# Performance work log

Hardware: AMD Instinct MI355X
Metric: run time of the kernel (lower is better)

## Reference

```python
import jax, jax.numpy as jnp
import numpy as np

EPS = 1e-6
N_HEADS, N_POINTS = 6, 4


def layer_norm(x, w, b):
    m = jnp.mean(x, -1, keepdims=True)
    v = jnp.mean((x - m) ** 2, -1, keepdims=True)
    return (x - m) * jax.lax.rsqrt(v + EPS) * w + b


def bilinear_sample(val, loc, Hl, Wl):
    # val: (B, nH, Hl*Wl, d); loc: (B, Lq, nH, P, 2) in [0,1]
    # matches F.grid_sample(mode='bilinear', padding='zeros', align_corners=False)
    B, nH, _, d = val.shape
    Lq, P = loc.shape[1], loc.shape[3]
    x = loc[..., 0] * Wl - 0.5
    y = loc[..., 1] * Hl - 0.5
    x0 = jnp.floor(x)
    y0 = jnp.floor(y)
    wx1 = x - x0
    wy1 = y - y0
    out = jnp.zeros((B, nH, Lq * P, d), val.dtype)
    corners = ((0, 0, (1 - wy1) * (1 - wx1)), (0, 1, (1 - wy1) * wx1),
               (1, 0, wy1 * (1 - wx1)), (1, 1, wy1 * wx1))
    for dy, dx, w in corners:
        xi = x0 + dx
        yi = y0 + dy
        valid = (xi >= 0) & (xi < Wl) & (yi >= 0) & (yi < Hl)
        xi_c = jnp.clip(xi, 0, Wl - 1).astype(jnp.int32)
        yi_c = jnp.clip(yi, 0, Hl - 1).astype(jnp.int32)
        idx = (yi_c * Wl + xi_c).transpose(0, 2, 1, 3).reshape(B, nH, Lq * P)
        g = jnp.take_along_axis(val, idx[..., None], axis=2)  # (B,nH,Lq*P,d)
        ww = jnp.where(valid, w, 0.0).transpose(0, 2, 1, 3).reshape(B, nH, Lq * P)
        out = out + g * ww[..., None]
    return out.reshape(B, nH, Lq, P, d).transpose(0, 2, 1, 3, 4)  # (B,Lq,nH,P,d)


def dwconv3x3(x, w, b):
    # x: (N, C, H, W); w: (C, 1, 3, 3) depthwise
    y = jax.lax.conv_general_dilated(x, w, (1, 1), 'SAME',
                                     feature_group_count=w.shape[0],
                                     dimension_numbers=('NCHW', 'OIHW', 'NCHW'))
    return y + b[None, :, None, None]


def setup_inputs() -> dict:
    key = jax.random.key(0)
    ks = jax.random.split(key, 16)
    B, H, W, C = 8, 32, 32, 768
    Lq = 3 * H * W
    Hf = Wf = 64
    hidden = int(C * 0.25)
    s = 0.02
    inp = {
        'query': jax.random.normal(ks[0], (B, Lq, C), jnp.float32),
        'reference_points': jax.random.uniform(ks[1], (B, Lq, 1, 2), jnp.float32),
        'feat': jax.random.normal(ks[2], (B, Hf * Wf, C), jnp.float32),
        'spatial_shapes': jnp.array([[Hf, Wf]], jnp.int32),
        'level_start_index': jnp.zeros((1,), jnp.int32),
        'H': H, 'W': W,
        'qn_w': jnp.ones((C,)), 'qn_b': jnp.zeros((C,)),
        'fn_w': jnp.ones((C,)), 'fn_b': jnp.zeros((C,)),
        'so_w': jax.random.normal(ks[3], (C, N_HEADS * N_POINTS * 2)) * s,
        'so_b': jax.random.normal(ks[4], (N_HEADS * N_POINTS * 2,)) * s,
        'aw_w': jax.random.normal(ks[5], (C, N_HEADS * N_POINTS)) * s,
        'aw_b': jnp.zeros((N_HEADS * N_POINTS,)),
        'vp_w': jax.random.normal(ks[6], (C, C)) * s,
        'vp_b': jnp.zeros((C,)),
        'op_w': jax.random.normal(ks[7], (C, C)) * s,
        'op_b': jnp.zeros((C,)),
        'ffn_w': jnp.ones((C,)), 'ffn_b': jnp.zeros((C,)),
        'fc1_w': jax.random.normal(ks[8], (C, hidden)) * s,
        'fc1_b': jnp.zeros((hidden,)),
        'dw_w': jax.random.normal(ks[9], (hidden, 1, 3, 3)) * s,
        'dw_b': jnp.zeros((hidden,)),
        'fc2_w': jax.random.normal(ks[10], (hidden, C)) * s,
        'fc2_b': jnp.zeros((C,)),
    }
    return inp


def reference(query, reference_points, feat, spatial_shapes, level_start_index, H, W,
              qn_w, qn_b, fn_w, fn_b, so_w, so_b, aw_w, aw_b, vp_w, vp_b, op_w, op_b,
              ffn_w, ffn_b, fc1_w, fc1_b, dw_w, dw_b, fc2_w, fc2_b):
    B, Lq, C = query.shape
    nH, nP = N_HEADS, N_POINTS
    d = C // nH
    ss = np.asarray(spatial_shapes)
    Hl, Wl = int(ss[0, 0]), int(ss[0, 1])

    # --- MSDeformAttn (single level) ---
    q = layer_norm(query, qn_w, qn_b)
    f = layer_norm(feat, fn_w, fn_b)
    value = (f @ vp_w + vp_b).reshape(B, Hl * Wl, nH, d).transpose(0, 2, 1, 3)  # (B,nH,Lin,d)
    offs = (q @ so_w + so_b).reshape(B, Lq, nH, 1, nP, 2)
    aw = jax.nn.softmax((q @ aw_w + aw_b).reshape(B, Lq, nH, nP), axis=-1)
    normalizer = jnp.array([Wl, Hl], query.dtype)
    loc = reference_points[:, :, None, :, None, :] + offs / normalizer  # (B,Lq,nH,1,nP,2)
    sampled = bilinear_sample(value, loc[:, :, :, 0], Hl, Wl)           # (B,Lq,nH,nP,d)
    attn = (sampled * aw[..., None]).sum(3).reshape(B, Lq, C) @ op_w + op_b
    query = query + attn

    # --- ConvFFN (3 equal HxW chunks through shared depthwise conv) ---
    x = layer_norm(query, ffn_w, ffn_b) @ fc1_w + fc1_b  # (B, 3*H*W, hid)
    n = Lq // 3
    hid = fc1_w.shape[1]
    xc = x.reshape(B, 3, n, hid).transpose(0, 1, 3, 2).reshape(B * 3, hid, H, W)
    xc = dwconv3x3(xc, dw_w, dw_b)
    x = xc.reshape(B, 3, hid, n).transpose(0, 1, 3, 2).reshape(B, Lq, hid)
    x = jax.nn.gelu(x, approximate=False)
    x = x @ fc2_w + fc2_b
    return query + x
```

## Files before the change

### kernel.cpp

```cpp
#include <hip/hip_runtime.h>
#include <hip/hip_bf16.h>
#include <math.h>

typedef __hip_bfloat16 bf16;
typedef short bf16x8 __attribute__((ext_vector_type(8)));
typedef short bf16x4 __attribute__((ext_vector_type(4)));
typedef float f32x4 __attribute__((ext_vector_type(4)));

#define NB 8
#define LQ 3072
#define CC 768
#define NHEADS 6
#define NPTS 4
#define DHEAD 128
#define HLVL 64
#define WLVL 64
#define LIN 4096
#define HID 192
#define BLTOT 24576
#define FROWS 32768

__device__ __forceinline__ float bf2f(short u)
{ return __uint_as_float(((unsigned)(unsigned short)u) << 16); }

__global__ __launch_bounds__(256)
void ln_bf16_kernel(const float* __restrict__ x, const float* __restrict__ w,
                    const float* __restrict__ b, bf16* __restrict__ out)
{
    const int row = blockIdx.x;
    const int t = threadIdx.x;
    const float* xr = x + (size_t)row * CC;
    float v0 = xr[t], v1 = xr[t + 256], v2 = xr[t + 512];
    float s = v0 + v1 + v2;
    float ss = v0 * v0 + v1 * v1 + v2 * v2;
    #pragma unroll
    for (int o = 32; o > 0; o >>= 1) {
        s += __shfl_down(s, o);
        ss += __shfl_down(ss, o);
    }
    __shared__ float red[8];
    const int lane = t & 63, wv = t >> 6;
    if (lane == 0) { red[wv] = s; red[4 + wv] = ss; }
    __syncthreads();
    if (t == 0) {
        float S = red[0] + red[1] + red[2] + red[3];
        float SS = red[4] + red[5] + red[6] + red[7];
        float m = S * (1.f / CC);
        float var = SS * (1.f / CC) - m * m;
        red[0] = m; red[1] = rsqrtf(var + 1e-6f);
    }
    __syncthreads();
    const float m = red[0], rs = red[1];
    bf16* o = out + (size_t)row * CC;
    o[t]       = __float2bfloat16((v0 - m) * rs * w[t] + b[t]);
    o[t + 256] = __float2bfloat16((v1 - m) * rs * w[t + 256] + b[t + 256]);
    o[t + 512] = __float2bfloat16((v2 - m) * rs * w[t + 512] + b[t + 512]);
}

__global__ __launch_bounds__(256)
void ln_bf16in_kernel(const bf16* __restrict__ x, const float* __restrict__ w,
                      const float* __restrict__ b, bf16* __restrict__ out)
{
    const int row = blockIdx.x * 4 + (threadIdx.x >> 6);
    const int lane = threadIdx.x & 63;
    const bf16* xr = x + (size_t)row * CC;
    bf16x8 v8 = *(const bf16x8*)(xr + lane * 8);
    bf16x4 v4 = *(const bf16x4*)(xr + 512 + lane * 4);
    float v[12];
    #pragma unroll
    for (int j = 0; j < 8; ++j) v[j] = bf2f(v8[j]);
    #pragma unroll
    for (int j = 0; j < 4; ++j) v[8 + j] = bf2f(v4[j]);
    float s = 0.f, ss = 0.f;
    #pragma unroll
    for (int j = 0; j < 12; ++j) { s += v[j]; ss += v[j] * v[j]; }
    #pragma unroll
    for (int o = 32; o > 0; o >>= 1) {
        s += __shfl_down(s, o);
        ss += __shfl_down(ss, o);
    }
    s = __shfl(s, 0); ss = __shfl(ss, 0);
    const float m = s * (1.f / CC);
    const float rs = rsqrtf(ss * (1.f / CC) - m * m + 1e-6f);
    float wv[12], bv[12];
    *(float4*)&wv[0] = *(const float4*)&w[lane * 8];
    *(float4*)&wv[4] = *(const float4*)&w[lane * 8 + 4];
    *(float4*)&wv[8] = *(const float4*)&w[512 + lane * 4];
    *(float4*)&bv[0] = *(const float4*)&b[lane * 8];
    *(float4*)&bv[4] = *(const float4*)&b[lane * 8 + 4];
    *(float4*)&bv[8] = *(const float4*)&b[512 + lane * 4];
    bf16 o8[8], o4[4];
    #pragma unroll
    for (int j = 0; j < 8; ++j) o8[j] = __float2bfloat16((v[j] - m) * rs * wv[j] + bv[j]);
    #pragma unroll
    for (int j = 0; j < 4; ++j) o4[j] = __float2bfloat16((v[8 + j] - m) * rs * wv[8 + j] + bv[8 + j]);
    bf16* orow = out + (size_t)row * CC;
    *(bf16x8*)(orow + lane * 8) = *(bf16x8*)o8;
    *(bf16x4*)(orow + 512 + lane * 4) = *(bf16x4*)o4;
}

__global__ __launch_bounds__(256)
void wt_bf16_kernel(const float* __restrict__ src, bf16* __restrict__ dst, int K, int N)
{
    __shared__ float t[64][65];
    const int tn0 = blockIdx.x * 64, tk0 = blockIdx.y * 64;
    const int r = threadIdx.x >> 6, c = threadIdx.x & 63;
    #pragma unroll
    for (int i = 0; i < 16; ++i) {
        const int k = i * 4 + r;
        t[k][c] = src[(size_t)(tk0 + k) * N + tn0 + c];
    }
    __syncthreads();
    #pragma unroll
    for (int i = 0; i < 16; ++i) {
        const int n = i * 4 + r;
        dst[(size_t)(tn0 + n) * K + tk0 + c] = __float2bfloat16(t[c][n]);
    }
}

__global__ __launch_bounds__(256)
void build_dots_w(const float* __restrict__ so_w, const float* __restrict__ so_b,
                  const float* __restrict__ aw_w, const float* __restrict__ aw_b,
                  bf16* __restrict__ wt, float* __restrict__ db)
{
    int i = blockIdx.x * 256 + threadIdx.x;
    if (i < 128 * 768) {
        int n = i / 768, k = i - n * 768;
        float v = 0.f;
        if (n < 48) v = so_w[(size_t)k * 48 + n];
        else if (n < 72) v = aw_w[(size_t)k * 24 + (n - 48)];
        wt[i] = __float2bfloat16(v);
    }
    if (i < 128) {
        float bv = 0.f;
        if (i < 48) bv = so_b[i];
        else if (i < 72) bv = aw_b[i - 48];
        db[i] = bv;
    }
}

template<int N_>
__device__ __forceinline__ void wait_vmcnt()
{
    if constexpr (N_ == 0)      asm volatile("s_waitcnt vmcnt(0)" ::: "memory");
    else if constexpr (N_ == 4) asm volatile("s_waitcnt vmcnt(4)" ::: "memory");
    else if constexpr (N_ == 5) asm volatile("s_waitcnt vmcnt(5)" ::: "memory");
    else if constexpr (N_ == 6) asm volatile("s_waitcnt vmcnt(6)" ::: "memory");
    else if constexpr (N_ == 8) asm volatile("s_waitcnt vmcnt(8)" ::: "memory");
    else static_assert(N_ == 0, "add a vmcnt case");
}

template<int BM, int BN, int WM, int WN, int MODE>
__global__ __launch_bounds__(256)
void gemm_kernel(const bf16* __restrict__ A, const bf16* __restrict__ Bt,
                 const float* __restrict__ bias, const void* __restrict__ resv,
                 void* __restrict__ outv, int M, int N, int K)
{
    constexpr int WAVES_N = BN / WN;
    constexpr int FM = WM / 16, FN = WN / 16;
    constexpr int CWA = BM / 32;
    constexpr int CWB = BN / 32;
    constexpr int LPT = CWA + CWB;
    constexpr int ABYTES = BM * 256;
    constexpr int DBUF_BYTES = (BM + BN) * 256;
    constexpr int EPI_BYTES = BM * BN * 4;
    constexpr size_t SMEM_BYTES = DBUF_BYTES > EPI_BYTES ? DBUF_BYTES : EPI_BYTES;
    __shared__ __align__(16) char smem[SMEM_BYTES];
    bf16* sA = (bf16*)smem;
    bf16* sB = (bf16*)(smem + ABYTES);
    float* epi = (float*)smem;

    const int tid = threadIdx.x;
    const int lane = tid & 63;
    const int wave = tid >> 6;

    const int nwgx = gridDim.x;
    const int nwg = nwgx * gridDim.y;
    const int bid = blockIdx.y * nwgx + blockIdx.x;
    const int swz = (bid & 7) * (nwg >> 3) + (bid >> 3);
    const int m0 = (swz / nwgx) * BM;
    const int n0 = (swz % nwgx) * BN;

    const int wm = (wave / WAVES_N) * WM;
    const int wn = (wave % WAVES_N) * WN;

    const int srow = lane >> 3;
    const int scol = ((lane & 7) ^ srow) * 8;

    constexpr int GPR8 = BN / 8;
    constexpr int GPT8 = (BM * BN / 8) / 256;
    constexpr int QPR4 = BN / 4;
    constexpr int QPT4 = (BM * BN / 4) / 256;
    float4 pr0[GPT8], pr1[GPT8];
    bf16x4 prb[QPT4];
    if constexpr (MODE == 3) {
        const float* resf = (const float*)resv;
        #pragma unroll
        for (int k = 0; k < GPT8; ++k) {
            const int f = k * 256 + tid;
            const int rr = f / GPR8, cc = (f % GPR8) * 8;
            const size_t gidx = (size_t)(m0 + rr) * N + n0 + cc;
            pr0[k] = *(const float4*)&resf[gidx];
            pr1[k] = *(const float4*)&resf[gidx + 4];
        }
    }
    if constexpr (MODE == 4) {
        const bf16* resb = (const bf16*)resv;
        #pragma unroll
        for (int k = 0; k < QPT4; ++k) {
            const int f = k * 256 + tid;
            const int rr = f / QPR4, cc = (f % QPR4) * 4;
            prb[k] = *(const bf16x4*)&resb[(size_t)(m0 + rr) * N + n0 + cc];
        }
    }

#define STAGE(tt, half)                                                                            \
    { const int k0_ = (tt) * 64;                                                                   \
      _Pragma("unroll")                                                                            \
      for (int i_ = 0; i_ < CWA; ++i_) {                                                           \
        const int c_ = i_ * 4 + wave;                                                              \
        __builtin_amdgcn_global_load_lds(                                                          \
          (const __attribute__((address_space(1))) void*)(A + (size_t)(m0 + c_ * 8 + srow) * K + k0_ + scol), \
          (__attribute__((address_space(3))) void*)(sA + (half) * (BM * 64) + c_ * 512), 16, 0, 0); } \
      _Pragma("unroll")                                                                            \
      for (int i_ = 0; i_ < CWB; ++i_) {                                                           \
        const int c_ = i_ * 4 + wave;                                                              \
        __builtin_amdgcn_global_load_lds(                                                          \
          (const __attribute__((address_space(1))) void*)(Bt + (size_t)(n0 + c_ * 8 + srow) * K + k0_ + scol), \
          (__attribute__((address_space(3))) void*)(sB + (half) * (BN * 64) + c_ * 512), 16, 0, 0); } }

    f32x4 acc[FM][FN] = {};
    const int nt = K >> 6;

    STAGE(0, 0);
    STAGE(1, 1);

    for (int t = 0; t < nt; ++t) {
        const int half = t & 1;
        if (t + 1 < nt) wait_vmcnt<LPT>();
        else            wait_vmcnt<0>();
        __builtin_amdgcn_s_barrier();
        const bf16* cA = sA + half * (BM * 64);
        const bf16* cB = sB + half * (BN * 64);
        #pragma unroll
        for (int kki = 0; kki < 2; ++kki) {
            const int kslot = kki * 4 + (lane >> 4);
            bf16x8 aF[FM], bF[FN];
            #pragma unroll
            for (int i = 0; i < FM; ++i) {
                const int row = wm + i * 16 + (lane & 15);
                aF[i] = *(const bf16x8*)(&cA[row * 64 + ((kslot ^ (row & 7)) * 8)]);
            }
            #pragma unroll
            for (int j = 0; j < FN; ++j) {
                const int row = wn + j * 16 + (lane & 15);
                bF[j] = *(const bf16x8*)(&cB[row * 64 + ((kslot ^ (row & 7)) * 8)]);
            }
            #pragma unroll
            for (int i = 0; i < FM; ++i) {
                #pragma unroll
                for (int j = 0; j < FN; ++j)
                    acc[i][j] = __builtin_amdgcn_mfma_f32_16x16x32_bf16(aF[i], bF[j], acc[i][j], 0, 0, 0);
            }
        }
        asm volatile("s_waitcnt lgkmcnt(0)" ::: "memory");
        __builtin_amdgcn_s_barrier();
        if (t + 2 < nt) STAGE(t + 2, half);
    }
#undef STAGE

    #pragma unroll
    for (int j = 0; j < FN; ++j) {
        const int colL = wn + j * 16 + (lane & 15);
        const float bj = bias[n0 + colL];
        #pragma unroll
        for (int i = 0; i < FM; ++i) {
            #pragma unroll
            for (int r = 0; r < 4; ++r) {
                const int rowL = wm + i * 16 + ((lane >> 4) << 2) + r;
                const int addr = rowL * BN + ((((colL >> 2) ^ (rowL & 7)) << 2) | (colL & 3));
                epi[addr] = acc[i][j][r] + bj;
            }
        }
    }
    __syncthreads();

    if constexpr (MODE == 0 || MODE == 3) {
        #pragma unroll
        for (int k = 0; k < GPT8; ++k) {
            const int f = k * 256 + tid;
            const int rr = f / GPR8, cc = (f % GPR8) * 8;
            const int g0 = ((cc >> 2) ^ (rr & 7)) << 2;
            const int g1 = (((cc >> 2) + 1) ^ (rr & 7)) << 2;
            float4 v0 = *(const float4*)&epi[rr * BN + g0];
            float4 v1 = *(const float4*)&epi[rr * BN + g1];
            if constexpr (MODE == 3) {
                v0.x += pr0[k].x; v0.y += pr0[k].y; v0.z += pr0[k].z; v0.w += pr0[k].w;
                v1.x += pr1[k].x; v1.y += pr1[k].y; v1.z += pr1[k].z; v1.w += pr1[k].w;
            }
            bf16 tmp[8];
            tmp[0] = __float2bfloat16(v0.x); tmp[1] = __float2bfloat16(v0.y);
            tmp[2] = __float2bfloat16(v0.z); tmp[3] = __float2bfloat16(v0.w);
            tmp[4] = __float2bfloat16(v1.x); tmp[5] = __float2bfloat16(v1.y);
            tmp[6] = __float2bfloat16(v1.z); tmp[7] = __float2bfloat16(v1.w);
            *(bf16x8*)((bf16*)outv + (size_t)(m0 + rr) * N + n0 + cc) = *(bf16x8*)tmp;
        }
    } else {
        #pragma unroll
        for (int k = 0; k < QPT4; ++k) {
            const int f = k * 256 + tid;
            const int rr = f / QPR4, cc = (f % QPR4) * 4;
            const int gs = ((cc >> 2) ^ (rr & 7)) << 2;
            float4 v = *(const float4*)&epi[rr * BN + gs];
            if constexpr (MODE == 4) {
                v.x += bf2f(prb[k][0]); v.y += bf2f(prb[k][1]);
                v.z += bf2f(prb[k][2]); v.w += bf2f(prb[k][3]);
            }
            *(float4*)&((float*)outv)[(size_t)(m0 + rr) * N + n0 + cc] = v;
        }
    }
}

__global__ __launch_bounds__(256)
void locsoftmax_kernel(const float* __restrict__ dots, const float* __restrict__ refp,
                       float4* __restrict__ params)
{
    int i = blockIdx.x * 256 + threadIdx.x;
    if (i >= BLTOT * NHEADS) return;
    int bl = i / NHEADS, h = i - bl * NHEADS;
    const float* d = dots + (size_t)bl * 128;
    float rx = refp[(size_t)bl * 2], ry = refp[(size_t)bl * 2 + 1];
    float l0 = d[48 + h * 4 + 0], l1 = d[48 + h * 4 + 1];
    float l2 = d[48 + h * 4 + 2], l3 = d[48 + h * 4 + 3];
    float mx = fmaxf(fmaxf(l0, l1), fmaxf(l2, l3));
    float e0 = expf(l0 - mx), e1 = expf(l1 - mx), e2 = expf(l2 - mx), e3 = expf(l3 - mx);
    float inv = 1.f / (e0 + e1 + e2 + e3);
    float ee[4] = {e0, e1, e2, e3};
    #pragma unroll
    for (int p = 0; p < 4; ++p) {
        float ox = d[h * 8 + p * 2], oy = d[h * 8 + p * 2 + 1];
        params[(size_t)i * 4 + p] =
            make_float4(rx + ox * (1.f / WLVL), ry + oy * (1.f / HLVL), ee[p] * inv, 0.f);
    }
}

__global__ __launch_bounds__(256)
void sampler_kernel(const bf16* __restrict__ value, const float4* __restrict__ params,
                    bf16* __restrict__ attn_in)
{
    const int tid = threadIdx.x;
    const int g = blockIdx.x * 16 + (tid >> 4);
    const int lane16 = tid & 15;
    const int bl = g / NHEADS;
    const int h = g - bl * NHEADS;
    const int b = bl / LQ;
    const bf16* vh = value + (size_t)b * LIN * CC + h * DHEAD + lane16 * 8;

    int offs[16];
    float wgt[16];
    #pragma unroll
    for (int p = 0; p < NPTS; ++p) {
        float4 pr = params[(size_t)g * 4 + p];
        float x = pr.x * (float)WLVL - 0.5f;
        float y = pr.y * (float)HLVL - 0.5f;
        float x0f = floorf(x), y0f = floorf(y);
        float wx1 = x - x0f, wy1 = y - y0f;
        float wx0 = 1.f - wx1, wy0 = 1.f - wy1;
        int x0 = (int)x0f, y0 = (int)y0f;
        #pragma unroll
        for (int dy = 0; dy < 2; ++dy) {
            const int yi = y0 + dy;
            const int yc = min(max(yi, 0), HLVL - 1);
            const float wy = (dy ? wy1 : wy0) * ((yi >= 0 && yi < HLVL) ? pr.z : 0.f);
            #pragma unroll
            for (int dx = 0; dx < 2; ++dx) {
                const int xi = x0 + dx;
                const int xc = min(max(xi, 0), WLVL - 1);
                const int idx = p * 4 + dy * 2 + dx;
                offs[idx] = (yc * WLVL + xc) * CC;
                wgt[idx] = wy * (dx ? wx1 : wx0) * ((xi >= 0 && xi < WLVL) ? 1.f : 0.f);
            }
        }
    }
    bf16x8 v[16];
    #pragma unroll
    for (int i = 0; i < 16; ++i) v[i] = *(const bf16x8*)(vh + offs[i]);
    float acc[8] = {};
    #pragma unroll
    for (int i = 0; i < 16; ++i) {
        #pragma unroll
        for (int j = 0; j < 8; ++j)
            acc[j] += wgt[i] * bf2f(v[i][j]);
    }
    bf16 tmp[8];
    #pragma unroll
    for (int j = 0; j < 8; ++j) tmp[j] = __float2bfloat16(acc[j]);
    *(bf16x8*)(attn_in + (size_t)bl * CC + h * DHEAD + lane16 * 8) = *(bf16x8*)tmp;
}

__global__ __launch_bounds__(192)
void dwconv_gelu_kernel(const bf16* __restrict__ z, const float* __restrict__ dw_w,
                        const float* __restrict__ dw_b, bf16* __restrict__ g)
{
    const int tp = threadIdx.x / 48;
    const int tc = threadIdx.x % 48;
    const int m = blockIdx.x * 4 + tp;
    const int c = tc * 4;
    const int pix = m & 1023;
    const int h = pix >> 5, w = pix & 31;
    float acc[4];
    #pragma unroll
    for (int j = 0; j < 4; ++j) acc[j] = dw_b[c + j];
    #pragma unroll
    for (int dy = -1; dy <= 1; ++dy) {
        int hh2 = h + dy;
        if (hh2 < 0 || hh2 >= 32) continue;
        #pragma unroll
        for (int dx = -1; dx <= 1; ++dx) {
            int ww2 = w + dx;
            if (ww2 < 0 || ww2 >= 32) continue;
            bf16x4 vv = *(const bf16x4*)&z[(size_t)(m + dy * 32 + dx) * HID + c];
            #pragma unroll
            for (int j = 0; j < 4; ++j)
                acc[j] += bf2f(vv[j]) * dw_w[(c + j) * 9 + (dy + 1) * 3 + (dx + 1)];
        }
    }
    bf16 tmp[4];
    #pragma unroll
    for (int j = 0; j < 4; ++j) {
        float ge = acc[j] * 0.5f * (1.f + erff(acc[j] * 0.70710678118f));
        tmp[j] = __float2bfloat16(ge);
    }
    *(bf16x4*)&g[(size_t)m * HID + c] = *(bf16x4*)tmp;
}

extern "C" void kernel_launch(void* const* d_in, const int* in_sizes, int n_in,
                              void* d_out, int out_size, void* d_ws, size_t ws_size,
                              hipStream_t stream)
{
    const float* query = (const float*)d_in[0];
    const float* refp  = (const float*)d_in[1];
    const float* feat  = (const float*)d_in[2];
    const float* qn_w = (const float*)d_in[7];
    const float* qn_b = (const float*)d_in[8];
    const float* fn_w = (const float*)d_in[9];
    const float* fn_b = (const float*)d_in[10];
    const float* so_w = (const float*)d_in[11];
    const float* so_b = (const float*)d_in[12];
    const float* aw_w = (const float*)d_in[13];
    const float* aw_b = (const float*)d_in[14];
    const float* vp_w = (const float*)d_in[15];
    const float* vp_b = (const float*)d_in[16];
    const float* op_w = (const float*)d_in[17];
    const float* op_b = (const float*)d_in[18];
    const float* ffn_w = (const float*)d_in[19];
    const float* ffn_b = (const float*)d_in[20];
    const float* fc1_w = (const float*)d_in[21];
    const float* fc1_b = (const float*)d_in[22];
    const float* dw_w = (const float*)d_in[23];
    const float* dw_b = (const float*)d_in[24];
    const float* fc2_w = (const float*)d_in[25];
    const float* fc2_b = (const float*)d_in[26];
    float* out = (float*)d_out;

    if (ws_size < (size_t)125829632) return;
    char* ws = (char*)d_ws;
    bf16* vp_wt   = (bf16*)(ws + 0);
    bf16* op_wt   = (bf16*)(ws + 1179648);
    bf16* fc1_wt  = (bf16*)(ws + 2359296);
    bf16* fc2_wt  = (bf16*)(ws + 2654208);
    bf16* dots_wt = (bf16*)(ws + 2949120);
    float* dots_b = (float*)(ws + 3145728);
    char* paramsR = ws + 3146240;
    char* dotsR   = ws + 12583424;
    char* regA = ws + 25166336;
    char* regB = ws + 75497984;
    float4* params = (float4*)paramsR;
    bf16* g        = (bf16*)paramsR;
    float* dots_out = (float*)dotsR;
    bf16* z         = (bf16*)dotsR;
    bf16* f_ln    = (bf16*)regA;
    bf16* attn_in = (bf16*)regA;
    bf16* y       = (bf16*)regA;
    bf16* q_ln  = (bf16*)regB;
    bf16* value = (bf16*)regB;
    bf16* s_bf  = (bf16*)regB;

    wt_bf16_kernel<<<dim3(12, 12), 256, 0, stream>>>(vp_w, vp_wt, 768, 768);
    wt_bf16_kernel<<<dim3(12, 12), 256, 0, stream>>>(op_w, op_wt, 768, 768);
    wt_bf16_kernel<<<dim3(3, 12), 256, 0, stream>>>(fc1_w, fc1_wt, 768, 192);
    wt_bf16_kernel<<<dim3(12, 3), 256, 0, stream>>>(fc2_w, fc2_wt, 192, 768);
    build_dots_w<<<384, 256, 0, stream>>>(so_w, so_b, aw_w, aw_b, dots_wt, dots_b);

    ln_bf16_kernel<<<BLTOT, 256, 0, stream>>>(query, qn_w, qn_b, q_ln);
    gemm_kernel<32, 128, 16, 64, 2><<<dim3(1, BLTOT / 32), 256, 0, stream>>>(
        q_ln, dots_wt, dots_b, nullptr, dots_out, BLTOT, 128, 768);
    locsoftmax_kernel<<<(BLTOT * NHEADS + 255) / 256, 256, 0, stream>>>(dots_out, refp, params);
    ln_bf16_kernel<<<FROWS, 256, 0, stream>>>(feat, fn_w, fn_b, f_ln);
    gemm_kernel<128, 128, 64, 64, 0><<<dim3(6, FROWS / 128), 256, 0, stream>>>(
        f_ln, vp_wt, vp_b, nullptr, value, FROWS, 768, 768);
    sampler_kernel<<<(BLTOT * NHEADS) / 16, 256, 0, stream>>>(value, params, attn_in);
    gemm_kernel<64, 128, 32, 64, 3><<<dim3(6, BLTOT / 64), 256, 0, stream>>>(
        attn_in, op_wt, op_b, query, s_bf, BLTOT, 768, 768);

    ln_bf16in_kernel<<<BLTOT / 4, 256, 0, stream>>>(s_bf, ffn_w, ffn_b, y);
    gemm_kernel<64, 64, 16, 64, 0><<<dim3(3, BLTOT / 64), 256, 0, stream>>>(
        y, fc1_wt, fc1_b, nullptr, z, BLTOT, HID, 768);
    dwconv_gelu_kernel<<<BLTOT / 4, 192, 0, stream>>>(z, dw_w, dw_b, g);
    gemm_kernel<64, 128, 32, 64, 4><<<dim3(6, BLTOT / 64), 256, 0, stream>>>(
        g, fc2_wt, fc2_b, s_bf, out, BLTOT, 768, HID);
}
```

Baseline: 342.9 us.

## Fuse LayerNorm into GEMM prologues and softmax/location into dots epilogue

Adds an ln_gemm kernel that normalizes rows straight into shared memory as the A operand and streams the B tiles. It also applies the softmax and location computation in the epilogue for the offsets/attention-weight projection. The same kernel fuses the FFN LayerNorm into fc1. This removes the separate q_ln, y and dots intermediate buffers and their kernel launches. The feat LayerNorm moves to a one-wave-per-row kernel, and the sampler block order is swizzled for locality. In exchange the fused kernels hold a full 768-wide A tile in LDS, and the fc1 path redoes the LayerNorm for each N tile (3x), which may lower occupancy.

After: 327.2 us. 1.05x faster.

```diff
diff --git a/kernel.cpp b/kernel.cpp
--- a/kernel.cpp
+++ b/kernel.cpp
@@ -23,80 +23,48 @@
 __device__ __forceinline__ float bf2f(short u)
 { return __uint_as_float(((unsigned)(unsigned short)u) << 16); }
 
+template<int N_>
+__device__ __forceinline__ void wait_vmcnt()
+{
+    if constexpr (N_ == 0)      asm volatile("s_waitcnt vmcnt(0)" ::: "memory");
+    else if constexpr (N_ == 2) asm volatile("s_waitcnt vmcnt(2)" ::: "memory");
+    else if constexpr (N_ == 4) asm volatile("s_waitcnt vmcnt(4)" ::: "memory");
+    else if constexpr (N_ == 6) asm volatile("s_waitcnt vmcnt(6)" ::: "memory");
+    else if constexpr (N_ == 8) asm volatile("s_waitcnt vmcnt(8)" ::: "memory");
+    else static_assert(N_ == 0, "add a vmcnt case");
+}
+
 __global__ __launch_bounds__(256)
-void ln_bf16_kernel(const float* __restrict__ x, const float* __restrict__ w,
-                    const float* __restrict__ b, bf16* __restrict__ out)
-{
-    const int row = blockIdx.x;
-    const int t = threadIdx.x;
-    const float* xr = x + (size_t)row * CC;
-    float v0 = xr[t], v1 = xr[t + 256], v2 = xr[t + 512];
-    float s = v0 + v1 + v2;
-    float ss = v0 * v0 + v1 * v1 + v2 * v2;
-    #pragma unroll
-    for (int o = 32; o > 0; o >>= 1) {
-        s += __shfl_down(s, o);
-        ss += __shfl_down(ss, o);
-    }
-    __shared__ float red[8];
-    const int lane = t & 63, wv = t >> 6;
-    if (lane == 0) { red[wv] = s; red[4 + wv] = ss; }
-    __syncthreads();
-    if (t == 0) {
-        float S = red[0] + red[1] + red[2] + red[3];
-        float SS = red[4] + red[5] + red[6] + red[7];
-        float m = S * (1.f / CC);
-        float var = SS * (1.f / CC) - m * m;
-        red[0] = m; red[1] = rsqrtf(var + 1e-6f);
-    }
-    __syncthreads();
-    const float m = red[0], rs = red[1];
-    bf16* o = out + (size_t)row * CC;
-    o[t]       = __float2bfloat16((v0 - m) * rs * w[t] + b[t]);
-    o[t + 256] = __float2bfloat16((v1 - m) * rs * w[t + 256] + b[t + 256]);
-    o[t + 512] = __float2bfloat16((v2 - m) * rs * w[t + 512] + b[t + 512]);
-}
-
-__global__ __launch_bounds__(256)
-void ln_bf16in_kernel(const bf16* __restrict__ x, const float* __restrict__ w,
-                      const float* __restrict__ b, bf16* __restrict__ out)
+void ln_f32_wave_kernel(const float* __restrict__ x, const float* __restrict__ w,
+                        const float* __restrict__ b, bf16* __restrict__ out)
 {
     const int row = blockIdx.x * 4 + (threadIdx.x >> 6);
     const int lane = threadIdx.x & 63;
-    const bf16* xr = x + (size_t)row * CC;
-    bf16x8 v8 = *(const bf16x8*)(xr + lane * 8);
-    bf16x4 v4 = *(const bf16x4*)(xr + 512 + lane * 4);
-    float v[12];
-    #pragma unroll
-    for (int j = 0; j < 8; ++j) v[j] = bf2f(v8[j]);
-    #pragma unroll
-    for (int j = 0; j < 4; ++j) v[8 + j] = bf2f(v4[j]);
+    const f32x4* xr = (const f32x4*)(x + (size_t)row * CC);
+    f32x4 f0 = xr[lane], f1 = xr[64 + lane], f2 = xr[128 + lane];
     float s = 0.f, ss = 0.f;
     #pragma unroll
-    for (int j = 0; j < 12; ++j) { s += v[j]; ss += v[j] * v[j]; }
-    #pragma unroll
-    for (int o = 32; o > 0; o >>= 1) {
-        s += __shfl_down(s, o);
-        ss += __shfl_down(ss, o);
-    }
+    for (int k = 0; k < 4; ++k) {
+        s += f0[k] + f1[k] + f2[k];
+        ss += f0[k] * f0[k] + f1[k] * f1[k] + f2[k] * f2[k];
+    }
+    #pragma unroll
+    for (int o = 32; o > 0; o >>= 1) { s += __shfl_down(s, o); ss += __shfl_down(ss, o); }
     s = __shfl(s, 0); ss = __shfl(ss, 0);
     const float m = s * (1.f / CC);
     const float rs = rsqrtf(ss * (1.f / CC) - m * m + 1e-6f);
-    float wv[12], bv[12];
-    *(float4*)&wv[0] = *(const float4*)&w[lane * 8];
-    *(float4*)&wv[4] = *(const float4*)&w[lane * 8 + 4];
-    *(float4*)&wv[8] = *(const float4*)&w[512 + lane * 4];
-    *(float4*)&bv[0] = *(const float4*)&b[lane * 8];
-    *(float4*)&bv[4] = *(const float4*)&b[lane * 8 + 4];
-    *(float4*)&bv[8] = *(const float4*)&b[512 + lane * 4];
-    bf16 o8[8], o4[4];
-    #pragma unroll
-    for (int j = 0; j < 8; ++j) o8[j] = __float2bfloat16((v[j] - m) * rs * wv[j] + bv[j]);
-    #pragma unroll
-    for (int j = 0; j < 4; ++j) o4[j] = __float2bfloat16((v[8 + j] - m) * rs * wv[8 + j] + bv[8 + j]);
+    const f32x4* w4 = (const f32x4*)w;
+    const f32x4* b4 = (const f32x4*)b;
     bf16* orow = out + (size_t)row * CC;
-    *(bf16x8*)(orow + lane * 8) = *(bf16x8*)o8;
-    *(bf16x4*)(orow + 512 + lane * 4) = *(bf16x4*)o4;
+    #pragma unroll
+    for (int j = 0; j < 3; ++j) {
+        f32x4 fj = (j == 0) ? f0 : (j == 1) ? f1 : f2;
+        f32x4 wj = w4[j * 64 + lane], bj = b4[j * 64 + lane];
+        bf16 t4[4];
+        #pragma unroll
+        for (int k = 0; k < 4; ++k) t4[k] = __float2bfloat16((fj[k] - m) * rs * wj[k] + bj[k]);
+        *(bf16x4*)(orow + j * 256 + lane * 4) = *(bf16x4*)t4;
+    }
 }
 
 __global__ __launch_bounds__(256)
@@ -137,17 +105,6 @@
         else if (i < 72) bv = aw_b[i - 48];
         db[i] = bv;
     }
-}
-
-template<int N_>
-__device__ __forceinline__ void wait_vmcnt()
-{
-    if constexpr (N_ == 0)      asm volatile("s_waitcnt vmcnt(0)" ::: "memory");
-    else if constexpr (N_ == 4) asm volatile("s_waitcnt vmcnt(4)" ::: "memory");
-    else if constexpr (N_ == 5) asm volatile("s_waitcnt vmcnt(5)" ::: "memory");
-    else if constexpr (N_ == 6) asm volatile("s_waitcnt vmcnt(6)" ::: "memory");
-    else if constexpr (N_ == 8) asm volatile("s_waitcnt vmcnt(8)" ::: "memory");
-    else static_assert(N_ == 0, "add a vmcnt case");
 }
 
 template<int BM, int BN, int WM, int WN, int MODE>
@@ -321,26 +278,216 @@
     }
 }
 
+template<int BM, int BN, int WM, int WN, bool F32IN, int EPI>
 __global__ __launch_bounds__(256)
-void locsoftmax_kernel(const float* __restrict__ dots, const float* __restrict__ refp,
-                       float4* __restrict__ params)
-{
-    int i = blockIdx.x * 256 + threadIdx.x;
-    if (i >= BLTOT * NHEADS) return;
-    int bl = i / NHEADS, h = i - bl * NHEADS;
-    const float* d = dots + (size_t)bl * 128;
-    float rx = refp[(size_t)bl * 2], ry = refp[(size_t)bl * 2 + 1];
-    float l0 = d[48 + h * 4 + 0], l1 = d[48 + h * 4 + 1];
-    float l2 = d[48 + h * 4 + 2], l3 = d[48 + h * 4 + 3];
-    float mx = fmaxf(fmaxf(l0, l1), fmaxf(l2, l3));
-    float e0 = expf(l0 - mx), e1 = expf(l1 - mx), e2 = expf(l2 - mx), e3 = expf(l3 - mx);
-    float inv = 1.f / (e0 + e1 + e2 + e3);
-    float ee[4] = {e0, e1, e2, e3};
-    #pragma unroll
-    for (int p = 0; p < 4; ++p) {
-        float ox = d[h * 8 + p * 2], oy = d[h * 8 + p * 2 + 1];
-        params[(size_t)i * 4 + p] =
-            make_float4(rx + ox * (1.f / WLVL), ry + oy * (1.f / HLVL), ee[p] * inv, 0.f);
+void ln_gemm_kernel(const void* __restrict__ xv, const float* __restrict__ lnw,
+                    const float* __restrict__ lnb, const bf16* __restrict__ Bt,
+                    const float* __restrict__ bias, const float* __restrict__ refp,
+                    void* __restrict__ outv, int M, int N)
+{
+    constexpr int WAVES_N = BN / WN;
+    constexpr int FM = WM / 16, FN = WN / 16;
+    constexpr int CWB = BN / 32;
+    constexpr int RPW = BM / 4;
+    static_assert(BM * BN * 4 <= 2 * BN * 64 * 2, "epi must fit in sB");
+    __shared__ __align__(16) bf16 sA[BM * 768];
+    __shared__ __align__(16) char sBmem[2 * BN * 64 * 2];
+    bf16* sB = (bf16*)sBmem;
+    float* epi = (float*)sBmem;
+
+    const int tid = threadIdx.x;
+    const int lane = tid & 63;
+    const int wave = tid >> 6;
+
+    const int nwgx = gridDim.x;
+    const int nwg = nwgx * gridDim.y;
+    const int bid = blockIdx.y * nwgx + blockIdx.x;
+    const int swz = (bid & 7) * (nwg >> 3) + (bid >> 3);
+    const int m0 = (swz / nwgx) * BM;
+    const int n0 = (swz % nwgx) * BN;
+
+    const int wm = (wave / WAVES_N) * WM;
+    const int wn = (wave % WAVES_N) * WN;
+    const int srow = lane >> 3;
+    const int scol = ((lane & 7) ^ srow) * 8;
+
+#define STAGEB(tt, half)                                                                           \
+    { const int k0_ = (tt) * 64;                                                                   \
+      _Pragma("unroll")                                                                            \
+      for (int i_ = 0; i_ < CWB; ++i_) {                                                           \
+        const int c_ = i_ * 4 + wave;                                                              \
+        __builtin_amdgcn_global_load_lds(                                                          \
+          (const __attribute__((address_space(1))) void*)(Bt + (size_t)(n0 + c_ * 8 + srow) * 768 + k0_ + scol), \
+          (__attribute__((address_space(3))) void*)(sB + (half) * (BN * 64) + c_ * 512), 16, 0, 0); } }
+
+    STAGEB(0, 0);
+    STAGEB(1, 1);
+
+    if constexpr (F32IN) {
+        const f32x4* w4 = (const f32x4*)lnw;
+        const f32x4* b4 = (const f32x4*)lnb;
+        f32x4 wv0 = w4[lane], wv1 = w4[64 + lane], wv2 = w4[128 + lane];
+        f32x4 bv0 = b4[lane], bv1 = b4[64 + lane], bv2 = b4[128 + lane];
+        for (int rr = 0; rr < RPW; ++rr) {
+            const int r = wave * RPW + rr;
+            const f32x4* xr = (const f32x4*)((const float*)xv + (size_t)(m0 + r) * 768);
+            f32x4 f0 = xr[lane], f1 = xr[64 + lane], f2 = xr[128 + lane];
+            float s = 0.f, ss = 0.f;
+            #pragma unroll
+            for (int k = 0; k < 4; ++k) {
+                s += f0[k] + f1[k] + f2[k];
+                ss += f0[k] * f0[k] + f1[k] * f1[k] + f2[k] * f2[k];
+            }
+            #pragma unroll
+            for (int o = 32; o > 0; o >>= 1) { s += __shfl_down(s, o); ss += __shfl_down(ss, o); }
+            s = __shfl(s, 0); ss = __shfl(ss, 0);
+            const float mn = s * (1.f / 768);
+            const float rs = rsqrtf(ss * (1.f / 768) - mn * mn + 1e-6f);
+            const int rx7 = r & 7;
+            const int slot = (lane >> 1) & 7;
+            const int off = (lane & 1) * 4;
+            #pragma unroll
+            for (int j = 0; j < 3; ++j) {
+                f32x4 fj = (j == 0) ? f0 : (j == 1) ? f1 : f2;
+                f32x4 wj = (j == 0) ? wv0 : (j == 1) ? wv1 : wv2;
+                f32x4 bj = (j == 0) ? bv0 : (j == 1) ? bv1 : bv2;
+                bf16 t4[4];
+                #pragma unroll
+                for (int k = 0; k < 4; ++k)
+                    t4[k] = __float2bfloat16((fj[k] - mn) * rs * wj[k] + bj[k]);
+                const int kt = j * 4 + (lane >> 4);
+                *(bf16x4*)&sA[r * 768 + kt * 64 + ((slot ^ rx7) << 3) + off] = *(bf16x4*)t4;
+            }
+        }
+    } else {
+        const f32x4* w4 = (const f32x4*)lnw;
+        const f32x4* b4 = (const f32x4*)lnb;
+        f32x4 w80 = w4[lane * 2], w81 = w4[lane * 2 + 1], w44 = w4[128 + lane];
+        f32x4 b80 = b4[lane * 2], b81 = b4[lane * 2 + 1], b44 = b4[128 + lane];
+        for (int rr = 0; rr < RPW; ++rr) {
+            const int r = wave * RPW + rr;
+            const bf16* xr = (const bf16*)xv + (size_t)(m0 + r) * 768;
+            bf16x8 v8 = *(const bf16x8*)(xr + lane * 8);
+            bf16x4 v4 = *(const bf16x4*)(xr + 512 + lane * 4);
+            float f[12];
+            #pragma unroll
+            for (int k = 0; k < 8; ++k) f[k] = bf2f(v8[k]);
+            #pragma unroll
+            for (int k = 0; k < 4; ++k) f[8 + k] = bf2f(v4[k]);
+            float s = 0.f, ss = 0.f;
+            #pragma unroll
+            for (int k = 0; k < 12; ++k) { s += f[k]; ss += f[k] * f[k]; }
+            #pragma unroll
+            for (int o = 32; o > 0; o >>= 1) { s += __shfl_down(s, o); ss += __shfl_down(ss, o); }
+            s = __shfl(s, 0); ss = __shfl(ss, 0);
+            const float mn = s * (1.f / 768);
+            const float rs = rsqrtf(ss * (1.f / 768) - mn * mn + 1e-6f);
+            const int rx7 = r & 7;
+            bf16 t8[8];
+            #pragma unroll
+            for (int k = 0; k < 4; ++k) t8[k] = __float2bfloat16((f[k] - mn) * rs * w80[k] + b80[k]);
+            #pragma unroll
+            for (int k = 0; k < 4; ++k) t8[4 + k] = __float2bfloat16((f[4 + k] - mn) * rs * w81[k] + b81[k]);
+            *(bf16x8*)&sA[r * 768 + (lane >> 3) * 64 + (((lane & 7) ^ rx7) << 3)] = *(bf16x8*)t8;
+            bf16 t4[4];
+            #pragma unroll
+            for (int k = 0; k < 4; ++k) t4[k] = __float2bfloat16((f[8 + k] - mn) * rs * w44[k] + b44[k]);
+            *(bf16x4*)&sA[r * 768 + (8 + (lane >> 4)) * 64 + ((((lane >> 1) & 7) ^ rx7) << 3) + (lane & 1) * 4]
+                = *(bf16x4*)t4;
+        }
+    }
+    asm volatile("s_waitcnt lgkmcnt(0)" ::: "memory");
+
+    f32x4 acc[FM][FN] = {};
+    for (int t = 0; t < 12; ++t) {
+        const int half = t & 1;
+        if (t + 1 < 12) wait_vmcnt<CWB>();
+        else            wait_vmcnt<0>();
+        __builtin_amdgcn_s_barrier();
+        const bf16* cB = sB + half * (BN * 64);
+        #pragma unroll
+        for (int kki = 0; kki < 2; ++kki) {
+            const int kslot = kki * 4 + (lane >> 4);
+            bf16x8 aF[FM], bF[FN];
+            #pragma unroll
+            for (int i = 0; i < FM; ++i) {
+                const int row = wm + i * 16 + (lane & 15);
+                aF[i] = *(const bf16x8*)(&sA[row * 768 + t * 64 + ((kslot ^ (row & 7)) * 8)]);
+            }
+            #pragma unroll
+            for (int j = 0; j < FN; ++j) {
+                const int row = wn + j * 16 + (lane & 15);
+                bF[j] = *(const bf16x8*)(&cB[row * 64 + ((kslot ^ (row & 7)) * 8)]);
+            }
+            #pragma unroll
+            for (int i = 0; i < FM; ++i) {
+                #pragma unroll
+                for (int j = 0; j < FN; ++j)
+                    acc[i][j] = __builtin_amdgcn_mfma_f32_16x16x32_bf16(aF[i], bF[j], acc[i][j], 0, 0, 0);
+            }
+        }
+        asm volatile("s_waitcnt lgkmcnt(0)" ::: "memory");
+        __builtin_amdgcn_s_barrier();
+        if (t + 2 < 12) STAGEB(t + 2, half);
+    }
+#undef STAGEB
+
+    #pragma unroll
+    for (int j = 0; j < FN; ++j) {
+        const int colL = wn + j * 16 + (lane & 15);
+        const float bj = bias[n0 + colL];
+        #pragma unroll
+        for (int i = 0; i < FM; ++i) {
+            #pragma unroll
+            for (int r = 0; r < 4; ++r) {
+                const int rowL = wm + i * 16 + ((lane >> 4) << 2) + r;
+                const int addr = rowL * BN + ((((colL >> 2) ^ (rowL & 7)) << 2) | (colL & 3));
+                epi[addr] = acc[i][j][r] + bj;
+            }
+        }
+    }
+    __syncthreads();
+
+    if constexpr (EPI == 1) {
+        if (tid < BM * NHEADS) {
+            const int rowL = tid & (BM - 1);
+            const int h = tid / BM;
+            auto erd = [&](int col) -> float {
+                return epi[rowL * BN + ((((col >> 2) ^ (rowL & 7)) << 2) | (col & 3))];
+            };
+            float l0 = erd(48 + h * 4 + 0), l1 = erd(48 + h * 4 + 1);
+            float l2 = erd(48 + h * 4 + 2), l3 = erd(48 + h * 4 + 3);
+            float mx = fmaxf(fmaxf(l0, l1), fmaxf(l2, l3));
+            float e0 = expf(l0 - mx), e1 = expf(l1 - mx), e2 = expf(l2 - mx), e3 = expf(l3 - mx);
+            float inv = 1.f / (e0 + e1 + e2 + e3);
+            float ee[4] = {e0, e1, e2, e3};
+            const float rx = refp[(size_t)(m0 + rowL) * 2];
+            const float ry = refp[(size_t)(m0 + rowL) * 2 + 1];
+            float4* pp = (float4*)outv + ((size_t)(m0 + rowL) * NHEADS + h) * 4;
+            #pragma unroll
+            for (int p = 0; p < 4; ++p) {
+                float ox = erd(h * 8 + p * 2), oy = erd(h * 8 + p * 2 + 1);
+                pp[p] = make_float4(rx + ox * (1.f / WLVL), ry + oy * (1.f / HLVL), ee[p] * inv, 0.f);
+            }
+        }
+    } else {
+        constexpr int GPR8 = BN / 8;
+        constexpr int GPT8 = (BM * BN / 8) / 256;
+        #pragma unroll
+        for (int k = 0; k < GPT8; ++k) {
+            const int f = k * 256 + tid;
+            const int rr = f / GPR8, cc = (f % GPR8) * 8;
+            const int g0 = ((cc >> 2) ^ (rr & 7)) << 2;
+            const int g1 = (((cc >> 2) + 1) ^ (rr & 7)) << 2;
+            float4 v0 = *(const float4*)&epi[rr * BN + g0];
+            float4 v1 = *(const float4*)&epi[rr * BN + g1];
+            bf16 tmp[8];
+            tmp[0] = __float2bfloat16(v0.x); tmp[1] = __float2bfloat16(v0.y);
+            tmp[2] = __float2bfloat16(v0.z); tmp[3] = __float2bfloat16(v0.w);
+            tmp[4] = __float2bfloat16(v1.x); tmp[5] = __float2bfloat16(v1.y);
+            tmp[6] = __float2bfloat16(v1.z); tmp[7] = __float2bfloat16(v1.w);
+            *(bf16x8*)((bf16*)outv + (size_t)(m0 + rr) * N + n0 + cc) = *(bf16x8*)tmp;
+        }
     }
 }
 
@@ -349,7 +496,9 @@
                     bf16* __restrict__ attn_in)
 {
     const int tid = threadIdx.x;
-    const int g = blockIdx.x * 16 + (tid >> 4);
+    const int cpx = gridDim.x >> 3;
+    const int gblk = (blockIdx.x & 7) * cpx + (blockIdx.x >> 3);
+    const int g = gblk * 16 + (tid >> 4);
     const int lane16 = tid & 15;
     const int bl = g / NHEADS;
     const int h = g - bl * NHEADS;
@@ -477,12 +626,9 @@
     char* regB = ws + 75497984;
     float4* params = (float4*)paramsR;
     bf16* g        = (bf16*)paramsR;
-    float* dots_out = (float*)dotsR;
-    bf16* z         = (bf16*)dotsR;
+    bf16* z        = (bf16*)dotsR;
     bf16* f_ln    = (bf16*)regA;
     bf16* attn_in = (bf16*)regA;
-    bf16* y       = (bf16*)regA;
-    bf16* q_ln  = (bf16*)regB;
     bf16* value = (bf16*)regB;
     bf16* s_bf  = (bf16*)regB;
 
@@ -492,20 +638,17 @@
     wt_bf16_kernel<<<dim3(12, 3), 256, 0, stream>>>(fc2_w, fc2_wt, 192, 768);
     build_dots_w<<<384, 256, 0, stream>>>(so_w, so_b, aw_w, aw_b, dots_wt, dots_b);
 
-    ln_bf16_kernel<<<BLTOT, 256, 0, stream>>>(query, qn_w, qn_b, q_ln);
-    gemm_kernel<32, 128, 16, 64, 2><<<dim3(1, BLTOT / 32), 256, 0, stream>>>(
-        q_ln, dots_wt, dots_b, nullptr, dots_out, BLTOT, 128, 768);
-    locsoftmax_kernel<<<(BLTOT * NHEADS + 255) / 256, 256, 0, stream>>>(dots_out, refp, params);
-    ln_bf16_kernel<<<FROWS, 256, 0, stream>>>(feat, fn_w, fn_b, f_ln);
+    ln_gemm_kernel<32, 128, 16, 64, true, 1><<<dim3(1, BLTOT / 32), 256, 0, stream>>>(
+        query, qn_w, qn_b, dots_wt, dots_b, refp, params, BLTOT, 128);
+    ln_f32_wave_kernel<<<FROWS / 4, 256, 0, stream>>>(feat, fn_w, fn_b, f_ln);
     gemm_kernel<128, 128, 64, 64, 0><<<dim3(6, FROWS / 128), 256, 0, stream>>>(
         f_ln, vp_wt, vp_b, nullptr, value, FROWS, 768, 768);
     sampler_kernel<<<(BLTOT * NHEADS) / 16, 256, 0, stream>>>(value, params, attn_in);
     gemm_kernel<64, 128, 32, 64, 3><<<dim3(6, BLTOT / 64), 256, 0, stream>>>(
         attn_in, op_wt, op_b, query, s_bf, BLTOT, 768, 768);
 
-    ln_bf16in_kernel<<<BLTOT / 4, 256, 0, stream>>>(s_bf, ffn_w, ffn_b, y);
-    gemm_kernel<64, 64, 16, 64, 0><<<dim3(3, BLTOT / 64), 256, 0, stream>>>(
-        y, fc1_wt, fc1_b, nullptr, z, BLTOT, HID, 768);
+    ln_gemm_kernel<32, 64, 32, 16, false, 0><<<dim3(3, BLTOT / 32), 256, 0, stream>>>(
+        s_bf, ffn_w, ffn_b, fc1_wt, fc1_b, nullptr, z, BLTOT, HID);
     dwconv_gelu_kernel<<<BLTOT / 4, 192, 0, stream>>>(z, dw_w, dw_b, g);
     gemm_kernel<64, 128, 32, 64, 4><<<dim3(6, BLTOT / 64), 256, 0, stream>>>(
         g, fc2_wt, fc2_b, s_bf, out, BLTOT, 768, HID);
```
